# Optimization experiments

Measured on AMD Instinct MI355X. Metric: run time of the kernel, lower is better.

Reference implementation:

```python
import jax, jax.numpy as jnp
import numpy as np

N = 100000      # nodes
E = 640000      # edges
VOCAB = 100     # Embedding(num_embeddings=100)
EMB = 10        # embed_dim
H = 128         # GCN hidden width


def gcn_conv(x, W, b, src, dst, n):
    """PyG GCNConv: linear (no bias) -> add self loops -> sym-normalized scatter-add -> +bias."""
    x = x @ W                                  # [n, out]
    loop = jnp.arange(n, dtype=src.dtype)
    src2 = jnp.concatenate([src, loop])        # [E+n]
    dst2 = jnp.concatenate([dst, loop])
    deg = jax.ops.segment_sum(jnp.ones_like(dst2, dtype=x.dtype), dst2, num_segments=n)
    dinv = jnp.where(deg > 0, jax.lax.rsqrt(deg), 0.0)
    norm = dinv[src2] * dinv[dst2]             # [E+n]
    out = jax.ops.segment_sum(x[src2] * norm[:, None], dst2, num_segments=n)
    return out + b


def setup_inputs() -> dict:
    key = jax.random.key(0)
    ks = jax.random.split(key, 9)
    x = jax.random.randint(ks[0], (N, 1), 0, VOCAB, dtype=jnp.int32)
    edge_index = jax.random.randint(ks[1], (2, E), 0, N, dtype=jnp.int32)
    batch = jnp.zeros((N,), dtype=jnp.int32)
    emb = jax.random.normal(ks[2], (VOCAB, EMB), dtype=jnp.float32)
    W1 = jax.random.normal(ks[3], (EMB, H), dtype=jnp.float32) * 0.1
    b1 = jnp.zeros((H,), dtype=jnp.float32)
    W2 = jax.random.normal(ks[4], (H, H), dtype=jnp.float32) * 0.1
    b2 = jnp.zeros((H,), dtype=jnp.float32)
    W3 = jax.random.normal(ks[5], (H, 1), dtype=jnp.float32) * 0.1
    b3 = jnp.zeros((1,), dtype=jnp.float32)
    return {"x": x, "edge_index": edge_index, "batch": batch,
            "emb": emb, "W1": W1, "b1": b1, "W2": W2, "b2": b2, "W3": W3, "b3": b3}


def reference(x, edge_index, batch, emb, W1, b1, W2, b2, W3, b3):
    # eval mode: dropout(p=0.5) is identity
    h = emb[x[:, 0]]                           # [N, EMB] embedding lookup + squeeze
    src, dst = edge_index[0], edge_index[1]
    n = h.shape[0]
    h = jax.nn.relu(gcn_conv(h, W1, b1, src, dst, n))   # [N, 128]
    h = jax.nn.relu(gcn_conv(h, W2, b2, src, dst, n))   # [N, 128]
    out = jax.nn.sigmoid((h @ W3 + b3).reshape(-1))      # [N]
    return out
```

## Files before the change

kernel.cpp:

```cpp
#include <hip/hip_runtime.h>
#include <math.h>

#define HDIM 128
#define EMBD 10
#define CAP  32
#define ZSTRIDE 136

typedef __attribute__((ext_vector_type(8))) short short8;
typedef __attribute__((ext_vector_type(8))) unsigned short ushort8;
typedef __attribute__((ext_vector_type(4))) float float4a;
typedef __attribute__((ext_vector_type(2))) float float2a;
typedef __attribute__((ext_vector_type(2))) unsigned uint2a;

__device__ inline ushort bf16_rne(float f) {
    unsigned u = __float_as_uint(f);
    unsigned r = (u + 0x7fffu + ((u >> 16) & 1u)) >> 16;
    return (ushort)r;
}
__device__ inline float bf16_to_f(ushort u) {
    return __uint_as_float(((unsigned)u) << 16);
}

__global__ void k_prep(const float* __restrict__ emb, const float* __restrict__ W1,
                       const float* __restrict__ W2, ushort* __restrict__ Tb,
                       ushort* __restrict__ W2t, int* __restrict__ cnt,
                       int N, int vocab) {
    int t = blockIdx.x * 256 + threadIdx.x;
    if (t < N) cnt[t] = 0;
    if (t < vocab * HDIM) {
        int c = t >> 7, f = t & 127;
        float s = 0.f;
#pragma unroll
        for (int k = 0; k < EMBD; ++k) s += emb[c * EMBD + k] * W1[k * HDIM + f];
        Tb[t] = bf16_rne(s);
    }
    if (t < HDIM * HDIM) {
        int n = t >> 7, k = t & 127;
        W2t[t] = bf16_rne(W2[k * HDIM + n]);
    }
}

__global__ void k_fill(const int* __restrict__ src, const int* __restrict__ dst,
                       int* __restrict__ cnt, int* __restrict__ slot, int E) {
    int e = blockIdx.x * blockDim.x + threadIdx.x;
    if (e >= E) return;
    int d = dst[e];
    int p = atomicAdd(&cnt[d], 1);
    if (p < CAP) slot[(size_t)d * CAP + p] = src[e];
}

__global__ void k_meta(const int* __restrict__ x, const int* __restrict__ cnt,
                       unsigned* __restrict__ meta, int N) {
    int v = blockIdx.x * 256 + threadIdx.x;
    if (v >= N) return;
    meta[v] = ((unsigned)x[v] << 16) | (unsigned)bf16_rne(rsqrtf((float)cnt[v] + 1.0f));
}

__global__ __launch_bounds__(512) void k_gather1(const int* __restrict__ slot,
                                                 const int* __restrict__ cnt,
                                                 const unsigned* __restrict__ meta,
                                                 const ushort* __restrict__ Tb,
                                                 const float* __restrict__ b1,
                                                 unsigned char* __restrict__ Ap,
                                                 int N, int vocab) {
    __shared__ ushort TbL[100 * HDIM];
    int n8 = (vocab * HDIM) >> 3;
    for (int i = threadIdx.x; i < n8; i += 512)
        ((ushort8*)TbL)[i] = ((const ushort8*)Tb)[i];
    __syncthreads();

    int tid = blockIdx.x * 512 + threadIdx.x;
    int v = tid >> 4, q = tid & 15;
    if (v >= N) return;
    int deg = cnt[v];
    int m = min(deg, CAP);
    float dv = rsqrtf((float)deg + 1.0f);
    int total = m + 1;
    const int* slotv = slot + (size_t)v * CAP;

    float acc[8] = {0.f, 0.f, 0.f, 0.f, 0.f, 0.f, 0.f, 0.f};
    for (int base = 0; base < total; base += 8) {
        int4 sa = *(const int4*)(slotv + base);
        int4 sb = *(const int4*)(slotv + base + 4);
        int sv[8] = {sa.x, sa.y, sa.z, sa.w, sb.x, sb.y, sb.z, sb.w};
        const unsigned* mp[8];
#pragma unroll
        for (int t = 0; t < 8; ++t) {
            int idx = base + t;
            mp[t] = meta + ((idx < m) ? sv[t] : v);
        }
        unsigned m0, m1, m2, m3, m4, m5, m6, m7;
        asm volatile(
            "global_load_dword %0, %8, off\n\t"
            "global_load_dword %1, %9, off\n\t"
            "global_load_dword %2, %10, off\n\t"
            "global_load_dword %3, %11, off\n\t"
            "global_load_dword %4, %12, off\n\t"
            "global_load_dword %5, %13, off\n\t"
            "global_load_dword %6, %14, off\n\t"
            "global_load_dword %7, %15, off\n\t"
            "s_waitcnt vmcnt(0)"
            : "=&v"(m0), "=&v"(m1), "=&v"(m2), "=&v"(m3),
              "=&v"(m4), "=&v"(m5), "=&v"(m6), "=&v"(m7)
            : "v"(mp[0]), "v"(mp[1]), "v"(mp[2]), "v"(mp[3]),
              "v"(mp[4]), "v"(mp[5]), "v"(mp[6]), "v"(mp[7]));
        unsigned mm[8] = {m0, m1, m2, m3, m4, m5, m6, m7};
#pragma unroll
        for (int t = 0; t < 8; ++t) {
            float wt = (base + t <= m) ? bf16_to_f((ushort)(mm[t] & 0xffffu)) : 0.f;
            ushort8 y = *(const ushort8*)&TbL[(mm[t] >> 16) * HDIM + q * 8];
#pragma unroll
            for (int k = 0; k < 8; ++k) acc[k] += wt * bf16_to_f(y[k]);
        }
    }
    float4 bb0 = *(const float4*)(b1 + q * 8);
    float4 bb1 = *(const float4*)(b1 + q * 8 + 4);
    float bb[8] = {bb0.x, bb0.y, bb0.z, bb0.w, bb1.x, bb1.y, bb1.z, bb1.w};
    float o[8];
#pragma unroll
    for (int k = 0; k < 8; ++k)
        o[k] = dv * fmaxf(dv * acc[k] + bb[k], 0.f);
    unsigned lo = __builtin_amdgcn_cvt_pk_fp8_f32(o[0], o[1], 0u, false);
    lo = __builtin_amdgcn_cvt_pk_fp8_f32(o[2], o[3], lo, true);
    unsigned hi = __builtin_amdgcn_cvt_pk_fp8_f32(o[4], o[5], 0u, false);
    hi = __builtin_amdgcn_cvt_pk_fp8_f32(o[6], o[7], hi, true);
    uint2 ow = make_uint2(lo, hi);
    *(uint2*)(Ap + (size_t)v * HDIM + q * 8) = ow;
}

__global__ __launch_bounds__(256, 8) void k_conv2(const int* __restrict__ slot,
                                                  const int* __restrict__ cnt,
                                                  const unsigned char* __restrict__ Ap,
                                                  const ushort* __restrict__ W2t,
                                                  const float* __restrict__ b2,
                                                  const float* __restrict__ W3,
                                                  const float* __restrict__ b3,
                                                  float* __restrict__ out, int N) {
    __shared__ ushort Z[16 * ZSTRIDE];
    __shared__ float pbuf[4][16];
    int tid = threadIdx.x;
    int g = tid >> 4, q = tid & 15;
    int v0 = blockIdx.x * 16;
    int v = min(v0 + g, N - 1);

    int deg = cnt[v];
    int m = min(deg, CAP);
    float dv = rsqrtf((float)deg + 1.0f);
    int total = m + 1;
    const int* slotv = slot + (size_t)v * CAP;
    const unsigned char* aq = Ap + q * 8;

    float acc[8] = {0.f, 0.f, 0.f, 0.f, 0.f, 0.f, 0.f, 0.f};
    for (int base = 0; base < total; base += 8) {
        int4 sa = *(const int4*)(slotv + base);
        int4 sb = *(const int4*)(slotv + base + 4);
        int sv[8] = {sa.x, sa.y, sa.z, sa.w, sb.x, sb.y, sb.z, sb.w};
        const unsigned char* pp[8];
#pragma unroll
        for (int t = 0; t < 8; ++t) {
            int idx = base + t;
            int s = (idx < m) ? sv[t] : v;
            pp[t] = aq + (size_t)s * HDIM;
        }
        uint2a r0, r1, r2, r3, r4, r5, r6, r7;
        asm volatile(
            "global_load_dwordx2 %0, %8, off\n\t"
            "global_load_dwordx2 %1, %9, off\n\t"
            "global_load_dwordx2 %2, %10, off\n\t"
            "global_load_dwordx2 %3, %11, off\n\t"
            "global_load_dwordx2 %4, %12, off\n\t"
            "global_load_dwordx2 %5, %13, off\n\t"
            "global_load_dwordx2 %6, %14, off\n\t"
            "global_load_dwordx2 %7, %15, off\n\t"
            "s_waitcnt vmcnt(0)"
            : "=&v"(r0), "=&v"(r1), "=&v"(r2), "=&v"(r3),
              "=&v"(r4), "=&v"(r5), "=&v"(r6), "=&v"(r7)
            : "v"(pp[0]), "v"(pp[1]), "v"(pp[2]), "v"(pp[3]),
              "v"(pp[4]), "v"(pp[5]), "v"(pp[6]), "v"(pp[7]));
        uint2a rr[8] = {r0, r1, r2, r3, r4, r5, r6, r7};
#pragma unroll
        for (int t = 0; t < 8; ++t) {
            float wt = (base + t <= m) ? 1.f : 0.f;
            float2a f01 = __builtin_amdgcn_cvt_pk_f32_fp8(rr[t][0], false);
            float2a f23 = __builtin_amdgcn_cvt_pk_f32_fp8(rr[t][0], true);
            float2a f45 = __builtin_amdgcn_cvt_pk_f32_fp8(rr[t][1], false);
            float2a f67 = __builtin_amdgcn_cvt_pk_f32_fp8(rr[t][1], true);
            acc[0] += wt * f01.x; acc[1] += wt * f01.y;
            acc[2] += wt * f23.x; acc[3] += wt * f23.y;
            acc[4] += wt * f45.x; acc[5] += wt * f45.y;
            acc[6] += wt * f67.x; acc[7] += wt * f67.y;
        }
    }
    ushort8 z;
#pragma unroll
    for (int k = 0; k < 8; ++k) z[k] = bf16_rne(dv * acc[k]);
    *(ushort8*)&Z[g * ZSTRIDE + q * 8] = z;
    __syncthreads();

    int lane = tid & 63, w = tid >> 6;
    int l15 = lane & 15, g4 = lane >> 4;
    short8 af[4];
#pragma unroll
    for (int kt = 0; kt < 4; ++kt)
        af[kt] = *(const short8*)&Z[l15 * ZSTRIDE + kt * 32 + g4 * 8];

    float pr[4] = {0.f, 0.f, 0.f, 0.f};
#pragma unroll
    for (int i = 0; i < 2; ++i) {
        int nt = w * 2 + i;
        int col = nt * 16 + l15;
        const ushort* bp = W2t + (size_t)col * HDIM + g4 * 8;
        float4a accD = {0.f, 0.f, 0.f, 0.f};
#pragma unroll
        for (int kt = 0; kt < 4; ++kt) {
            short8 bf = *(const short8*)(bp + kt * 32);
            accD = __builtin_amdgcn_mfma_f32_16x16x32_bf16(af[kt], bf, accD, 0, 0, 0);
        }
        float bc = b2[col], wc = W3[col];
#pragma unroll
        for (int r = 0; r < 4; ++r)
            pr[r] += fmaxf(accD[r] + bc, 0.f) * wc;
    }
#pragma unroll
    for (int off = 1; off < 16; off <<= 1) {
#pragma unroll
        for (int r = 0; r < 4; ++r) pr[r] += __shfl_xor(pr[r], off, 16);
    }
    if (l15 == 0) {
#pragma unroll
        for (int r = 0; r < 4; ++r) pbuf[w][g4 * 4 + r] = pr[r];
    }
    __syncthreads();
    if (tid < 16) {
        int row = tid;
        float s = pbuf[0][row] + pbuf[1][row] + pbuf[2][row] + pbuf[3][row];
        int vr = v0 + row;
        if (vr < N) out[vr] = 1.f / (1.f + expf(-(s + b3[0])));
    }
}

extern "C" void kernel_launch(void* const* d_in, const int* in_sizes, int n_in,
                              void* d_out, int out_size, void* d_ws, size_t ws_size,
                              hipStream_t stream) {
    const int*   x    = (const int*)d_in[0];
    const int*   ei   = (const int*)d_in[1];
    const float* emb  = (const float*)d_in[3];
    const float* W1   = (const float*)d_in[4];
    const float* b1   = (const float*)d_in[5];
    const float* W2   = (const float*)d_in[6];
    const float* b2   = (const float*)d_in[7];
    const float* W3   = (const float*)d_in[8];
    const float* b3   = (const float*)d_in[9];
    float*       out  = (float*)d_out;

    int N = in_sizes[0];
    int E = in_sizes[1] / 2;
    int vocab = in_sizes[3] / EMBD;
    const int* src = ei;
    const int* dst = ei + E;

    char* w = (char*)d_ws;
    ushort*        Tb   = (ushort*)w;         w += (size_t)vocab * HDIM * 2;
    unsigned char* Ap   = (unsigned char*)w;  w += (size_t)N * HDIM;
    ushort*        W2t  = (ushort*)w;         w += (size_t)HDIM * HDIM * 2;
    int*           cnt  = (int*)w;            w += (size_t)N * 4;
    unsigned*      meta = (unsigned*)w;       w += (size_t)N * 4;
    int*           slot = (int*)w;            w += (size_t)N * CAP * 4 + 64;

    int prep_elems = N;
    if (vocab * HDIM > prep_elems) prep_elems = vocab * HDIM;
    if (HDIM * HDIM > prep_elems) prep_elems = HDIM * HDIM;
    k_prep<<<(prep_elems + 255) / 256, 256, 0, stream>>>(emb, W1, W2, Tb, W2t, cnt, N, vocab);
    k_fill<<<(E + 255) / 256, 256, 0, stream>>>(src, dst, cnt, slot, E);
    k_meta<<<(N + 255) / 256, 256, 0, stream>>>(x, cnt, meta, N);

    int g1blocks = (int)(((long long)N * 16 + 511) / 512);
    k_gather1<<<g1blocks, 512, 0, stream>>>(slot, cnt, meta, Tb, b1, Ap, N, vocab);

    int cblocks = (N + 15) / 16;
    k_conv2<<<cblocks, 256, 0, stream>>>(slot, cnt, Ap, W2t, b2, W3, b3, out, N);
}
```

Measured before the change: 179.1 us.

## Bucket nodes by degree into a permutation to balance gather workloads

k_meta now splits nodes into low-degree (at most 7) and high-degree buckets using two atomic counters and writes a permutation, low-degree nodes at the front and high-degree ones at the back. Both gather kernels process nodes in permutation order, so the 16-lane groups in a wavefront see similar degrees and the 8-wide neighbor loop diverges less. The cost is two contended global atomics per node, an extra indirection per node, and scattered writes: Ap rows land in permuted order and the output is written through perm.

```diff
diff --git a/kernel.cpp b/kernel.cpp
--- a/kernel.cpp
+++ b/kernel.cpp
@@ -5,6 +5,7 @@
 #define EMBD 10
 #define CAP  32
 #define ZSTRIDE 136
+#define DEGLO 7
 
 typedef __attribute__((ext_vector_type(8))) short short8;
 typedef __attribute__((ext_vector_type(8))) unsigned short ushort8;
@@ -24,9 +25,10 @@
 __global__ void k_prep(const float* __restrict__ emb, const float* __restrict__ W1,
                        const float* __restrict__ W2, ushort* __restrict__ Tb,
                        ushort* __restrict__ W2t, int* __restrict__ cnt,
-                       int N, int vocab) {
+                       int* __restrict__ bc, int N, int vocab) {
     int t = blockIdx.x * 256 + threadIdx.x;
     if (t < N) cnt[t] = 0;
+    if (t < 2) bc[t] = 0;
     if (t < vocab * HDIM) {
         int c = t >> 7, f = t & 127;
         float s = 0.f;
@@ -50,15 +52,22 @@
 }
 
 __global__ void k_meta(const int* __restrict__ x, const int* __restrict__ cnt,
-                       unsigned* __restrict__ meta, int N) {
+                       unsigned* __restrict__ meta, int* __restrict__ perm,
+                       int* __restrict__ bc, int N) {
     int v = blockIdx.x * 256 + threadIdx.x;
     if (v >= N) return;
-    meta[v] = ((unsigned)x[v] << 16) | (unsigned)bf16_rne(rsqrtf((float)cnt[v] + 1.0f));
+    int c = cnt[v];
+    meta[v] = ((unsigned)x[v] << 16) | (unsigned)bf16_rne(rsqrtf((float)c + 1.0f));
+    int pos;
+    if (c <= DEGLO) pos = atomicAdd(&bc[0], 1);
+    else            pos = N - 1 - atomicAdd(&bc[1], 1);
+    perm[pos] = v;
 }
 
 __global__ __launch_bounds__(512) void k_gather1(const int* __restrict__ slot,
                                                  const int* __restrict__ cnt,
                                                  const unsigned* __restrict__ meta,
+                                                 const int* __restrict__ perm,
                                                  const ushort* __restrict__ Tb,
                                                  const float* __restrict__ b1,
                                                  unsigned char* __restrict__ Ap,
@@ -70,8 +79,9 @@
     __syncthreads();
 
     int tid = blockIdx.x * 512 + threadIdx.x;
-    int v = tid >> 4, q = tid & 15;
-    if (v >= N) return;
+    int vi = tid >> 4, q = tid & 15;
+    if (vi >= N) return;
+    int v = perm[vi];
     int deg = cnt[v];
     int m = min(deg, CAP);
     float dv = rsqrtf((float)deg + 1.0f);
@@ -130,6 +140,7 @@
 
 __global__ __launch_bounds__(256, 8) void k_conv2(const int* __restrict__ slot,
                                                   const int* __restrict__ cnt,
+                                                  const int* __restrict__ perm,
                                                   const unsigned char* __restrict__ Ap,
                                                   const ushort* __restrict__ W2t,
                                                   const float* __restrict__ b2,
@@ -141,7 +152,7 @@
     int tid = threadIdx.x;
     int g = tid >> 4, q = tid & 15;
     int v0 = blockIdx.x * 16;
-    int v = min(v0 + g, N - 1);
+    int v = perm[min(v0 + g, N - 1)];
 
     int deg = cnt[v];
     int m = min(deg, CAP);
@@ -235,7 +246,7 @@
         int row = tid;
         float s = pbuf[0][row] + pbuf[1][row] + pbuf[2][row] + pbuf[3][row];
         int vr = v0 + row;
-        if (vr < N) out[vr] = 1.f / (1.f + expf(-(s + b3[0])));
+        if (vr < N) out[perm[vr]] = 1.f / (1.f + expf(-(s + b3[0])));
     }
 }
 
@@ -265,18 +276,20 @@
     ushort*        W2t  = (ushort*)w;         w += (size_t)HDIM * HDIM * 2;
     int*           cnt  = (int*)w;            w += (size_t)N * 4;
     unsigned*      meta = (unsigned*)w;       w += (size_t)N * 4;
-    int*           slot = (int*)w;            w += (size_t)N * CAP * 4 + 64;
+    int*           perm = (int*)w;            w += (size_t)N * 4;
+    int*           bc   = (int*)w;            w += 16 * 4;
+    int*           slot = (int*)w;            w += (size_t)N * CAP * 4 + 128;
 
     int prep_elems = N;
     if (vocab * HDIM > prep_elems) prep_elems = vocab * HDIM;
     if (HDIM * HDIM > prep_elems) prep_elems = HDIM * HDIM;
-    k_prep<<<(prep_elems + 255) / 256, 256, 0, stream>>>(emb, W1, W2, Tb, W2t, cnt, N, vocab);
+    k_prep<<<(prep_elems + 255) / 256, 256, 0, stream>>>(emb, W1, W2, Tb, W2t, cnt, bc, N, vocab);
     k_fill<<<(E + 255) / 256, 256, 0, stream>>>(src, dst, cnt, slot, E);
-    k_meta<<<(N + 255) / 256, 256, 0, stream>>>(x, cnt, meta, N);
+    k_meta<<<(N + 255) / 256, 256, 0, stream>>>(x, cnt, meta, perm, bc, N);
 
     int g1blocks = (int)(((long long)N * 16 + 511) / 512);
-    k_gather1<<<g1blocks, 512, 0, stream>>>(slot, cnt, meta, Tb, b1, Ap, N, vocab);
+    k_gather1<<<g1blocks, 512, 0, stream>>>(slot, cnt, meta, perm, Tb, b1, Ap, N, vocab);
 
     int cblocks = (N + 15) / 16;
-    k_conv2<<<cblocks, 256, 0, stream>>>(slot, cnt, Ap, W2t, b2, W3, b3, out, N);
-}
+    k_conv2<<<cblocks, 256, 0, stream>>>(slot, cnt, perm, Ap, W2t, b2, W3, b3, out, N);
+}
```

Result: slower. 212.8 us (+18.8%).
